# Performance work log

Hardware: AMD Instinct MI355X
Metric: run time of the kernel (lower is better)

## Reference

```python
import jax, jax.numpy as jnp
import numpy as np
import math

E = 1024
H = 16
D = E // H  # head_dim = 64
B, T = 2, 2048


def setup_inputs() -> dict:
    key = jax.random.key(0)
    ks = jax.random.split(key, 10)
    s_in = 1.0 / math.sqrt(E)
    s_hd = 1.0 / math.sqrt(D)
    return {
        "hidden_states": jax.random.normal(ks[0], (B, T, E), dtype=jnp.float32),
        # stacked per-head Linear weights (torch Linear: y = x @ W.T + b)
        "Wq": jax.random.uniform(ks[1], (H, E, D), jnp.float32, -s_in, s_in),
        "bq": jax.random.uniform(ks[2], (H, D), jnp.float32, -s_in, s_in),
        "Wk": jax.random.uniform(ks[3], (H, E, D), jnp.float32, -s_in, s_in),
        "bk": jax.random.uniform(ks[4], (H, D), jnp.float32, -s_in, s_in),
        "Wv": jax.random.uniform(ks[5], (H, E, D), jnp.float32, -s_in, s_in),
        "bv": jax.random.uniform(ks[6], (H, D), jnp.float32, -s_in, s_in),
        "Wo": jax.random.uniform(ks[7], (H, D, E), jnp.float32, -s_hd, s_hd),
        "bo": jax.random.uniform(ks[8], (H, E), jnp.float32, -s_hd, s_hd),
        "gate": jnp.ones((H,), dtype=jnp.float32),
    }


def reference(hidden_states, Wq, bq, Wk, bk, Wv, bv, Wo, bo, gate):
    # Batched per-head projections: [B,T,E] x [H,E,D] -> [B,H,T,D]
    Q = jnp.einsum("bte,hed->bhtd", hidden_states, Wq) + bq[None, :, None, :]
    K = jnp.einsum("bte,hed->bhtd", hidden_states, Wk) + bk[None, :, None, :]
    V = jnp.einsum("bte,hed->bhtd", hidden_states, Wv) + bv[None, :, None, :]
    scale = 1.0 / math.sqrt(D)
    scores = jnp.einsum("bhtd,bhsd->bhts", Q, K) * scale  # [B,H,T,T]
    weights = jax.nn.softmax(scores, axis=-1)
    attn = jnp.einsum("bhts,bhsd->bhtd", weights, V)  # [B,H,T,D]
    # Per-head output proj (bias included before gating), gated, summed over heads
    proj = jnp.einsum("bhtd,hde->bhte", attn, Wo) + bo[None, :, None, :]
    out = jnp.sum(proj * gate[None, :, None, None], axis=1)  # [B,T,E]
    return out
```

## Files before the change

### kernel.cpp

```cpp
#include <hip/hip_runtime.h>
#include <math.h>

#define E_DIM 1024
#define H_DIM 16
#define D_DIM 64
#define B_DIM 2
#define T_DIM 2048
#define M_TOT (B_DIM * T_DIM)

typedef __bf16 bf16_t;
typedef bf16_t bf16x4 __attribute__((ext_vector_type(4)));
typedef bf16_t bf16x8 __attribute__((ext_vector_type(8)));
typedef float f32x4 __attribute__((ext_vector_type(4)));

#define LOG2E_DIV8 0.18033688011112042f

__device__ __forceinline__ float fast_exp2(float x) {
#if __has_builtin(__builtin_amdgcn_exp2f)
    return __builtin_amdgcn_exp2f(x);
#else
    return __expf(x * 0.6931471805599453f);
#endif
}

__device__ __forceinline__ void load_lds16(const void* g, void* l) {
    __builtin_amdgcn_global_load_lds(
        (const __attribute__((address_space(1))) unsigned int*)g,
        (__attribute__((address_space(3))) unsigned int*)l, 16, 0, 0);
}

__global__ __launch_bounds__(256) void cast_x_kernel(const float* __restrict__ x,
                                                     bf16_t* __restrict__ xb) {
    size_t i = ((size_t)blockIdx.x * 256 + threadIdx.x) * 8;
    float4 a = *reinterpret_cast<const float4*>(x + i);
    float4 b = *reinterpret_cast<const float4*>(x + i + 4);
    bf16x8 o;
    o[0] = (bf16_t)a.x; o[1] = (bf16_t)a.y; o[2] = (bf16_t)a.z; o[3] = (bf16_t)a.w;
    o[4] = (bf16_t)b.x; o[5] = (bf16_t)b.y; o[6] = (bf16_t)b.z; o[7] = (bf16_t)b.w;
    *reinterpret_cast<bf16x8*>(xb + i) = o;
}

__global__ __launch_bounds__(256) void wqkv_t_kernel(
    const float* __restrict__ Wq, const float* __restrict__ Wk,
    const float* __restrict__ Wv, bf16_t* __restrict__ Wcat) {
    const int et = blockIdx.x, h = blockIdx.y, z = blockIdx.z;
    const float* W = z == 0 ? Wq : (z == 1 ? Wk : Wv);
    __shared__ float Tt[64][65];
    const int tid = threadIdx.x;
    const int r = tid >> 2, c4 = (tid & 3) * 16;
    const float* src = W + (size_t)h * 65536 + (size_t)(et * 64 + r) * 64 + c4;
    #pragma unroll
    for (int k = 0; k < 16; k += 4) {
        float4 v = *reinterpret_cast<const float4*>(src + k);
        Tt[r][c4 + k + 0] = v.x; Tt[r][c4 + k + 1] = v.y;
        Tt[r][c4 + k + 2] = v.z; Tt[r][c4 + k + 3] = v.w;
    }
    __syncthreads();
    bf16x8 o0, o1;
    #pragma unroll
    for (int k = 0; k < 8; ++k) o0[k] = (bf16_t)Tt[c4 + k][r];
    #pragma unroll
    for (int k = 0; k < 8; ++k) o1[k] = (bf16_t)Tt[c4 + 8 + k][r];
    bf16_t* dst = Wcat + ((size_t)(z * 16 + h) * 64 + r) * 1024 + et * 64 + c4;
    *reinterpret_cast<bf16x8*>(dst) = o0;
    *reinterpret_cast<bf16x8*>(dst + 8) = o1;
}

__global__ __launch_bounds__(256) void wo_t_kernel(const float* __restrict__ Wo,
                                                   const float* __restrict__ gate,
                                                   bf16_t* __restrict__ Wgt) {
    const int et = blockIdx.x, h = blockIdx.y;
    const float g = gate[h];
    __shared__ float Tt[64][65];
    const int tid = threadIdx.x;
    const int r = tid >> 2, c4 = (tid & 3) * 16;
    const float* src = Wo + (size_t)h * 65536 + (size_t)r * 1024 + et * 64 + c4;
    #pragma unroll
    for (int k = 0; k < 16; k += 4) {
        float4 v = *reinterpret_cast<const float4*>(src + k);
        Tt[r][c4 + k + 0] = v.x * g; Tt[r][c4 + k + 1] = v.y * g;
        Tt[r][c4 + k + 2] = v.z * g; Tt[r][c4 + k + 3] = v.w * g;
    }
    __syncthreads();
    bf16x8 o0, o1;
    #pragma unroll
    for (int k = 0; k < 8; ++k) o0[k] = (bf16_t)Tt[c4 + k][r];
    #pragma unroll
    for (int k = 0; k < 8; ++k) o1[k] = (bf16_t)Tt[c4 + 8 + k][r];
    bf16_t* dst = Wgt + (size_t)(et * 64 + r) * 1024 + h * 64 + c4;
    *reinterpret_cast<bf16x8*>(dst) = o0;
    *reinterpret_cast<bf16x8*>(dst + 8) = o1;
}

__global__ __launch_bounds__(256) void bias_sum_kernel(const float* __restrict__ bo,
                                                       const float* __restrict__ gate,
                                                       float* __restrict__ bsum) {
    int e = blockIdx.x * 256 + threadIdx.x;
    float s = 0.f;
    #pragma unroll
    for (int h = 0; h < H_DIM; ++h) s += gate[h] * bo[h * E_DIM + e];
    bsum[e] = s;
}

__global__ __launch_bounds__(256) void qk_gemm_kernel(
    const bf16_t* __restrict__ Xb, const bf16_t* __restrict__ Wcat,
    const float* __restrict__ bqp, const float* __restrict__ bkp,
    bf16_t* __restrict__ Qw, bf16_t* __restrict__ Kw) {
    const int p = blockIdx.x;
    const int l = (p & 7) * 64 + (p >> 3);
    const int mx = l & 31, ny = l >> 5;
    const int m0 = mx * 128, n0 = ny * 128;

    __shared__ bf16_t As[2][128][32];
    __shared__ bf16_t Bs[2][128][32];

    const int tid = threadIdx.x;
    const int lane = tid & 63, wid = tid >> 6;
    const int wr = wid >> 1, wc = wid & 1;
    const int lr = lane & 15, lg = lane >> 4;
    const int srow = lane >> 2, scol = (lane & 3) * 8;

    f32x4 acc[4][4] = {};

    #define STAGE_QK(buf, k0)                                                      \
        _Pragma("unroll")                                                          \
        for (int j = 0; j < 2; ++j) {                                              \
            load_lds16(Xb + (size_t)(m0 + wid * 32 + j * 16 + srow) * E_DIM + (k0) + scol, \
                       (char*)&As[buf][0][0] + wid * 2048 + j * 1024);             \
            load_lds16(Wcat + (size_t)(n0 + wid * 32 + j * 16 + srow) * E_DIM + (k0) + scol, \
                       (char*)&Bs[buf][0][0] + wid * 2048 + j * 1024);             \
        }

    STAGE_QK(0, 0);
    for (int t = 0; t < 32; ++t) {
        __syncthreads();
        if (t < 31) STAGE_QK((t + 1) & 1, (t + 1) * 32);
        const int b = t & 1;
        bf16x8 a[4], bb[4];
        #pragma unroll
        for (int i = 0; i < 4; ++i)
            a[i] = *reinterpret_cast<const bf16x8*>(&As[b][wr * 64 + i * 16 + lr][lg * 8]);
        #pragma unroll
        for (int j = 0; j < 4; ++j)
            bb[j] = *reinterpret_cast<const bf16x8*>(&Bs[b][wc * 64 + j * 16 + lr][lg * 8]);
        __builtin_amdgcn_s_setprio(1);
        #pragma unroll
        for (int j = 0; j < 4; ++j)
            #pragma unroll
            for (int i = 0; i < 4; ++i)
                acc[j][i] = __builtin_amdgcn_mfma_f32_16x16x32_bf16(bb[j], a[i], acc[j][i], 0, 0, 0);
        __builtin_amdgcn_s_setprio(0);
    }
    #undef STAGE_QK

    const int z = n0 >> 10;
    const float scale = (z == 0) ? LOG2E_DIV8 : 1.0f;
    const float* bias = (z == 0) ? bqp : bkp;
    bf16_t* Obase = (z == 0) ? Qw : Kw;
    const int b_idx = m0 >> 11;
    const int t00 = m0 & (T_DIM - 1);

    #pragma unroll
    for (int j = 0; j < 4; ++j) {
        const int n = n0 + wc * 64 + j * 16 + lg * 4;
        const int h = (n >> 6) & 15;
        const int dbase = (n & 63);
        const float4 bv4 = *reinterpret_cast<const float4*>(&bias[n & 1023]);
        bf16_t* O = Obase + (size_t)(b_idx * H_DIM + h) * T_DIM * 64;
        #pragma unroll
        for (int i = 0; i < 4; ++i) {
            const int t = t00 + wr * 64 + i * 16 + lr;
            bf16x4 t4;
            #pragma unroll
            for (int r = 0; r < 4; ++r)
                t4[r] = (bf16_t)((acc[j][i][r] + (&bv4.x)[r]) * scale);
            *reinterpret_cast<bf16x4*>(&O[(size_t)t * 64 + dbase]) = t4;
        }
    }
}

__global__ __launch_bounds__(256) void v_gemm_kernel(
    const bf16_t* __restrict__ Xb, const bf16_t* __restrict__ Wcat,
    const float* __restrict__ bvp, bf16_t* __restrict__ Vtw) {
    const int p = blockIdx.x;
    const int l = (p & 7) * 32 + (p >> 3);
    const int mx = l & 31, ny = l >> 5;
    const int m0 = mx * 128, n0 = ny * 128;
    const bf16_t* Wv = Wcat + (size_t)2048 * E_DIM;

    __shared__ bf16_t As[2][128][32];
    __shared__ bf16_t Bs[2][128][32];

    const int tid = threadIdx.x;
    const int lane = tid & 63, wid = tid >> 6;
    const int wr = wid >> 1, wc = wid & 1;
    const int lr = lane & 15, lg = lane >> 4;
    const int srow = lane >> 2, scol = (lane & 3) * 8;

    f32x4 acc[4][4] = {};

    #define STAGE_V(buf, k0)                                                       \
        _Pragma("unroll")                                                          \
        for (int j = 0; j < 2; ++j) {                                              \
            load_lds16(Xb + (size_t)(m0 + wid * 32 + j * 16 + srow) * E_DIM + (k0) + scol, \
                       (char*)&As[buf][0][0] + wid * 2048 + j * 1024);             \
            load_lds16(Wv + (size_t)(n0 + wid * 32 + j * 16 + srow) * E_DIM + (k0) + scol, \
                       (char*)&Bs[buf][0][0] + wid * 2048 + j * 1024);             \
        }

    STAGE_V(0, 0);
    for (int t = 0; t < 32; ++t) {
        __syncthreads();
        if (t < 31) STAGE_V((t + 1) & 1, (t + 1) * 32);
        const int b = t & 1;
        bf16x8 a[4], bb[4];
        #pragma unroll
        for (int i = 0; i < 4; ++i)
            a[i] = *reinterpret_cast<const bf16x8*>(&As[b][wr * 64 + i * 16 + lr][lg * 8]);
        #pragma unroll
        for (int j = 0; j < 4; ++j)
            bb[j] = *reinterpret_cast<const bf16x8*>(&Bs[b][wc * 64 + j * 16 + lr][lg * 8]);
        __builtin_amdgcn_s_setprio(1);
        #pragma unroll
        for (int i = 0; i < 4; ++i)
            #pragma unroll
            for (int j = 0; j < 4; ++j)
                acc[i][j] = __builtin_amdgcn_mfma_f32_16x16x32_bf16(a[i], bb[j], acc[i][j], 0, 0, 0);
        __builtin_amdgcn_s_setprio(0);
    }
    #undef STAGE_V

    const int b_idx = m0 >> 11;
    const int t00 = m0 & (T_DIM - 1);
    #pragma unroll
    for (int j = 0; j < 4; ++j) {
        const int n = n0 + wc * 64 + j * 16 + lr;
        const int h = (n >> 6) & 15;
        const int d = n & 63;
        const float bval = bvp[n];
        bf16_t* O = Vtw + (size_t)(b_idx * H_DIM + h) * 64 * T_DIM + (size_t)d * T_DIM;
        #pragma unroll
        for (int i = 0; i < 4; ++i) {
            const int t = t00 + wr * 64 + i * 16 + lg * 4;
            bf16x4 t4;
            #pragma unroll
            for (int r = 0; r < 4; ++r) t4[r] = (bf16_t)(acc[i][j][r] + bval);
            *reinterpret_cast<bf16x4*>(&O[t]) = t4;
        }
    }
}

__global__ __launch_bounds__(512, 4) void attn_mfma_kernel(
    const bf16_t* __restrict__ Q, const bf16_t* __restrict__ K,
    const bf16_t* __restrict__ Vt, bf16_t* __restrict__ Aw) {
    const int p = blockIdx.x;
    const int l = (p & 7) * 64 + (p >> 3);
    const int qx = l & 15, bh = l >> 4;
    const int b_idx = bh >> 4, h = bh & 15;
    const int q0 = qx * 128;
    const size_t base = (size_t)bh * T_DIM * 64;
    const int tstart = (qx & 1) << 3;

    __shared__ bf16_t Ks[128][72];
    __shared__ bf16_t Vs[64][136];
    __shared__ bf16_t Ps[8][16][136];

    const int tid = threadIdx.x;
    const int lane = tid & 63;
    const int wid = tid >> 6;
    const int lr = lane & 15, lg = lane >> 4;

    bf16x8 bq[2];
    #pragma unroll
    for (int kc = 0; kc < 2; ++kc)
        bq[kc] = *reinterpret_cast<const bf16x8*>(
            Q + base + (size_t)(q0 + wid * 16 + lr) * 64 + kc * 32 + lg * 8);

    const int kr = tid >> 2, kc0 = (tid & 3) * 16;
    const int vr = tid >> 3, vc0 = (tid & 7) * 16;

    bf16x8 kA, kB, vA, vB;
    {
        const bf16_t* ksrc = K + base + (size_t)(tstart * 128 + kr) * 64 + kc0;
        kA = *reinterpret_cast<const bf16x8*>(ksrc);
        kB = *reinterpret_cast<const bf16x8*>(ksrc + 8);
        const bf16_t* vsrc = Vt + base + (size_t)vr * T_DIM + tstart * 128 + vc0;
        vA = *reinterpret_cast<const bf16x8*>(vsrc);
        vB = *reinterpret_cast<const bf16x8*>(vsrc + 8);
        *reinterpret_cast<bf16x8*>(&Ks[kr][kc0])     = kA;
        *reinterpret_cast<bf16x8*>(&Ks[kr][kc0 + 8]) = kB;
        *reinterpret_cast<bf16x8*>(&Vs[vr][vc0])     = vA;
        *reinterpret_cast<bf16x8*>(&Vs[vr][vc0 + 8]) = vB;
    }
    __syncthreads();

    float mreg = -INFINITY, lrow = 0.f;
    f32x4 o[4] = {};

    for (int it = 0; it < 16; ++it) {
        const bool more = (it + 1) < 16;
        if (more) {
            const int nt = (tstart + it + 1) & 15;
            const bf16_t* ksrc = K + base + (size_t)(nt * 128 + kr) * 64 + kc0;
            kA = *reinterpret_cast<const bf16x8*>(ksrc);
            kB = *reinterpret_cast<const bf16x8*>(ksrc + 8);
            const bf16_t* vsrc = Vt + base + (size_t)vr * T_DIM + nt * 128 + vc0;
            vA = *reinterpret_cast<const bf16x8*>(vsrc);
            vB = *reinterpret_cast<const bf16x8*>(vsrc + 8);
        }

        f32x4 s[8] = {};
        __builtin_amdgcn_s_setprio(1);
        #pragma unroll
        for (int kb = 0; kb < 8; ++kb)
            #pragma unroll
            for (int kc = 0; kc < 2; ++kc) {
                bf16x8 ak = *reinterpret_cast<const bf16x8*>(&Ks[kb * 16 + lr][kc * 32 + lg * 8]);
                s[kb] = __builtin_amdgcn_mfma_f32_16x16x32_bf16(ak, bq[kc], s[kb], 0, 0, 0);
            }
        __builtin_amdgcn_s_setprio(0);

        float pmax = -INFINITY;
        #pragma unroll
        for (int kb = 0; kb < 8; ++kb)
            pmax = fmaxf(pmax,
                   fmaxf(fmaxf(s[kb][0], s[kb][1]), fmaxf(s[kb][2], s[kb][3])));
        pmax = fmaxf(pmax, __shfl_xor(pmax, 16));
        pmax = fmaxf(pmax, __shfl_xor(pmax, 32));

        if (__any(pmax > mreg + 11.5f)) {
            float newm = fmaxf(mreg, pmax);
            float alpha = fast_exp2(mreg - newm);
            mreg = newm;
            lrow *= alpha;
            #pragma unroll
            for (int db = 0; db < 4; ++db) o[db] *= alpha;
        }

        float rs = 0.f;
        #pragma unroll
        for (int kb = 0; kb < 8; ++kb) {
            bf16x4 t4;
            #pragma unroll
            for (int r = 0; r < 4; ++r) {
                float pv = fast_exp2(s[kb][r] - mreg);
                rs += pv;
                t4[r] = (bf16_t)pv;
            }
            *reinterpret_cast<bf16x4*>(&Ps[wid][lr][kb * 16 + lg * 4]) = t4;
        }
        rs += __shfl_xor(rs, 16);
        rs += __shfl_xor(rs, 32);
        lrow += rs;

        __builtin_amdgcn_s_setprio(1);
        #pragma unroll
        for (int sc = 0; sc < 4; ++sc) {
            bf16x8 bp = *reinterpret_cast<const bf16x8*>(&Ps[wid][lr][sc * 32 + lg * 8]);
            #pragma unroll
            for (int db = 0; db < 4; ++db) {
                bf16x8 av = *reinterpret_cast<const bf16x8*>(&Vs[db * 16 + lr][sc * 32 + lg * 8]);
                o[db] = __builtin_amdgcn_mfma_f32_16x16x32_bf16(av, bp, o[db], 0, 0, 0);
            }
        }
        __builtin_amdgcn_s_setprio(0);
        __syncthreads();

        if (more) {
            *reinterpret_cast<bf16x8*>(&Ks[kr][kc0])     = kA;
            *reinterpret_cast<bf16x8*>(&Ks[kr][kc0 + 8]) = kB;
            *reinterpret_cast<bf16x8*>(&Vs[vr][vc0])     = vA;
            *reinterpret_cast<bf16x8*>(&Vs[vr][vc0 + 8]) = vB;
        }
        __syncthreads();
    }

    const float linv = 1.f / lrow;
    const int t = q0 + wid * 16 + lr;
    const size_t rowbase = ((size_t)b_idx * T_DIM + t) * E_DIM + h * 64;
    #pragma unroll
    for (int db = 0; db < 4; ++db) {
        bf16x4 t4;
        #pragma unroll
        for (int r = 0; r < 4; ++r) t4[r] = (bf16_t)(o[db][r] * linv);
        *reinterpret_cast<bf16x4*>(&Aw[rowbase + db * 16 + lg * 4]) = t4;
    }
}

__global__ __launch_bounds__(256) void out_gemm_kernel(
    const bf16_t* __restrict__ Aw, const bf16_t* __restrict__ Wgt,
    const float* __restrict__ bsum, float* __restrict__ out) {
    const int p = blockIdx.x;
    const int l = (p & 7) * 32 + (p >> 3);
    const int mx = l & 31, ny = l >> 5;
    const int m0 = mx * 128, n0 = ny * 128;

    __shared__ bf16_t As[2][128][32];
    __shared__ bf16_t Bs[2][128][32];

    const int tid = threadIdx.x;
    const int lane = tid & 63, wid = tid >> 6;
    const int wr = wid >> 1, wc = wid & 1;
    const int lr = lane & 15, lg = lane >> 4;
    const int srow = lane >> 2, scol = (lane & 3) * 8;

    f32x4 acc[4][4] = {};

    #define STAGE_O(buf, k0)                                                       \
        _Pragma("unroll")                                                          \
        for (int j = 0; j < 2; ++j) {                                              \
            load_lds16(Aw + (size_t)(m0 + wid * 32 + j * 16 + srow) * E_DIM + (k0) + scol, \
                       (char*)&As[buf][0][0] + wid * 2048 + j * 1024);             \
            load_lds16(Wgt + (size_t)(n0 + wid * 32 + j * 16 + srow) * E_DIM + (k0) + scol, \
                       (char*)&Bs[buf][0][0] + wid * 2048 + j * 1024);             \
        }

    STAGE_O(0, 0);
    for (int t = 0; t < 32; ++t) {
        __syncthreads();
        if (t < 31) STAGE_O((t + 1) & 1, (t + 1) * 32);
        const int b = t & 1;
        bf16x8 a[4], bb[4];
        #pragma unroll
        for (int i = 0; i < 4; ++i)
            a[i] = *reinterpret_cast<const bf16x8*>(&As[b][wr * 64 + i * 16 + lr][lg * 8]);
        #pragma unroll
        for (int j = 0; j < 4; ++j)
            bb[j] = *reinterpret_cast<const bf16x8*>(&Bs[b][wc * 64 + j * 16 + lr][lg * 8]);
        __builtin_amdgcn_s_setprio(1);
        #pragma unroll
        for (int j = 0; j < 4; ++j)
            #pragma unroll
            for (int i = 0; i < 4; ++i)
                acc[j][i] = __builtin_amdgcn_mfma_f32_16x16x32_bf16(bb[j], a[i], acc[j][i], 0, 0, 0);
        __builtin_amdgcn_s_setprio(0);
    }
    #undef STAGE_O

    #pragma unroll
    for (int j = 0; j < 4; ++j) {
        const int e = n0 + wc * 64 + j * 16 + lg * 4;
        const float4 bs4 = *reinterpret_cast<const float4*>(&bsum[e]);
        #pragma unroll
        for (int i = 0; i < 4; ++i) {
            const int m = m0 + wr * 64 + i * 16 + lr;
            float4 o4;
            o4.x = acc[j][i][0] + bs4.x;
            o4.y = acc[j][i][1] + bs4.y;
            o4.z = acc[j][i][2] + bs4.z;
            o4.w = acc[j][i][3] + bs4.w;
            *reinterpret_cast<float4*>(&out[(size_t)m * E_DIM + e]) = o4;
        }
    }
}

extern "C" void kernel_launch(void* const* d_in, const int* in_sizes, int n_in,
                              void* d_out, int out_size, void* d_ws, size_t ws_size,
                              hipStream_t stream) {
    const float* hs   = (const float*)d_in[0];
    const float* Wq   = (const float*)d_in[1];
    const float* bq   = (const float*)d_in[2];
    const float* Wk   = (const float*)d_in[3];
    const float* bk   = (const float*)d_in[4];
    const float* Wv   = (const float*)d_in[5];
    const float* bv   = (const float*)d_in[6];
    const float* Wo   = (const float*)d_in[7];
    const float* bo   = (const float*)d_in[8];
    const float* gate = (const float*)d_in[9];
    float* out = (float*)d_out;

    const size_t NX = (size_t)M_TOT * E_DIM;
    const size_t NW = (size_t)H_DIM * D_DIM * E_DIM;
    bf16_t* p = (bf16_t*)d_ws;
    bf16_t* Xb   = p; p += NX;
    bf16_t* Wcat = p; p += 3 * NW;
    bf16_t* Wgt  = p; p += NW;
    bf16_t* Qw   = p; p += NX;
    bf16_t* Kw   = p; p += NX;
    bf16_t* Vtw  = p; p += NX;
    bf16_t* Aw   = p; p += NX;
    float*  bsum = (float*)p;

    cast_x_kernel<<<dim3(NX / 2048), 256, 0, stream>>>(hs, Xb);
    wqkv_t_kernel<<<dim3(16, 16, 3), 256, 0, stream>>>(Wq, Wk, Wv, Wcat);
    wo_t_kernel<<<dim3(16, 16), 256, 0, stream>>>(Wo, gate, Wgt);
    bias_sum_kernel<<<dim3(4), 256, 0, stream>>>(bo, gate, bsum);

    qk_gemm_kernel<<<dim3(512), 256, 0, stream>>>(Xb, Wcat, bq, bk, Qw, Kw);
    v_gemm_kernel<<<dim3(256), 256, 0, stream>>>(Xb, Wcat, bv, Vtw);

    attn_mfma_kernel<<<dim3(512), 512, 0, stream>>>(Qw, Kw, Vtw, Aw);

    out_gemm_kernel<<<dim3(256), 256, 0, stream>>>(Aw, Wgt, bsum, out);
}
```

Measured before the change: 245.8 us.

## Merge prep kernels, fuse QKV GEMMs, single-buffer LDS, halve out-GEMM tile

Folds the four preprocessing kernels into one launch that branches on block index, and merges the QK and V projection GEMMs into a single 768-block launch. It also drops the LDS double-buffering in the GEMMs in favour of single-buffered loads with two barriers per step. The attention kernel's register prefetch and staggered start tile are removed, and the output GEMM moves to 128x64 tiles so it launches 512 blocks. The goal is less launch overhead and better occupancy and SM fill, at the cost of no longer overlapping global loads with MFMA compute.

```diff
diff --git a/kernel.cpp b/kernel.cpp
--- a/kernel.cpp
+++ b/kernel.cpp
@@ -29,90 +29,91 @@
         (__attribute__((address_space(3))) unsigned int*)l, 16, 0, 0);
 }
 
-__global__ __launch_bounds__(256) void cast_x_kernel(const float* __restrict__ x,
-                                                     bf16_t* __restrict__ xb) {
-    size_t i = ((size_t)blockIdx.x * 256 + threadIdx.x) * 8;
-    float4 a = *reinterpret_cast<const float4*>(x + i);
-    float4 b = *reinterpret_cast<const float4*>(x + i + 4);
-    bf16x8 o;
-    o[0] = (bf16_t)a.x; o[1] = (bf16_t)a.y; o[2] = (bf16_t)a.z; o[3] = (bf16_t)a.w;
-    o[4] = (bf16_t)b.x; o[5] = (bf16_t)b.y; o[6] = (bf16_t)b.z; o[7] = (bf16_t)b.w;
-    *reinterpret_cast<bf16x8*>(xb + i) = o;
-}
-
-__global__ __launch_bounds__(256) void wqkv_t_kernel(
+__global__ __launch_bounds__(256) void prep_kernel(
+    const float* __restrict__ x,
     const float* __restrict__ Wq, const float* __restrict__ Wk,
-    const float* __restrict__ Wv, bf16_t* __restrict__ Wcat) {
-    const int et = blockIdx.x, h = blockIdx.y, z = blockIdx.z;
-    const float* W = z == 0 ? Wq : (z == 1 ? Wk : Wv);
+    const float* __restrict__ Wv, const float* __restrict__ Wo,
+    const float* __restrict__ bo, const float* __restrict__ gate,
+    bf16_t* __restrict__ Xb, bf16_t* __restrict__ Wcat,
+    bf16_t* __restrict__ Wgt, float* __restrict__ bsum) {
     __shared__ float Tt[64][65];
+    const int b = blockIdx.x;
     const int tid = threadIdx.x;
-    const int r = tid >> 2, c4 = (tid & 3) * 16;
-    const float* src = W + (size_t)h * 65536 + (size_t)(et * 64 + r) * 64 + c4;
-    #pragma unroll
-    for (int k = 0; k < 16; k += 4) {
-        float4 v = *reinterpret_cast<const float4*>(src + k);
-        Tt[r][c4 + k + 0] = v.x; Tt[r][c4 + k + 1] = v.y;
-        Tt[r][c4 + k + 2] = v.z; Tt[r][c4 + k + 3] = v.w;
-    }
-    __syncthreads();
-    bf16x8 o0, o1;
-    #pragma unroll
-    for (int k = 0; k < 8; ++k) o0[k] = (bf16_t)Tt[c4 + k][r];
-    #pragma unroll
-    for (int k = 0; k < 8; ++k) o1[k] = (bf16_t)Tt[c4 + 8 + k][r];
-    bf16_t* dst = Wcat + ((size_t)(z * 16 + h) * 64 + r) * 1024 + et * 64 + c4;
-    *reinterpret_cast<bf16x8*>(dst) = o0;
-    *reinterpret_cast<bf16x8*>(dst + 8) = o1;
-}
-
-__global__ __launch_bounds__(256) void wo_t_kernel(const float* __restrict__ Wo,
-                                                   const float* __restrict__ gate,
-                                                   bf16_t* __restrict__ Wgt) {
-    const int et = blockIdx.x, h = blockIdx.y;
-    const float g = gate[h];
-    __shared__ float Tt[64][65];
-    const int tid = threadIdx.x;
-    const int r = tid >> 2, c4 = (tid & 3) * 16;
-    const float* src = Wo + (size_t)h * 65536 + (size_t)r * 1024 + et * 64 + c4;
-    #pragma unroll
-    for (int k = 0; k < 16; k += 4) {
-        float4 v = *reinterpret_cast<const float4*>(src + k);
-        Tt[r][c4 + k + 0] = v.x * g; Tt[r][c4 + k + 1] = v.y * g;
-        Tt[r][c4 + k + 2] = v.z * g; Tt[r][c4 + k + 3] = v.w * g;
-    }
-    __syncthreads();
-    bf16x8 o0, o1;
-    #pragma unroll
-    for (int k = 0; k < 8; ++k) o0[k] = (bf16_t)Tt[c4 + k][r];
-    #pragma unroll
-    for (int k = 0; k < 8; ++k) o1[k] = (bf16_t)Tt[c4 + 8 + k][r];
-    bf16_t* dst = Wgt + (size_t)(et * 64 + r) * 1024 + h * 64 + c4;
-    *reinterpret_cast<bf16x8*>(dst) = o0;
-    *reinterpret_cast<bf16x8*>(dst + 8) = o1;
-}
-
-__global__ __launch_bounds__(256) void bias_sum_kernel(const float* __restrict__ bo,
-                                                       const float* __restrict__ gate,
-                                                       float* __restrict__ bsum) {
-    int e = blockIdx.x * 256 + threadIdx.x;
-    float s = 0.f;
-    #pragma unroll
-    for (int h = 0; h < H_DIM; ++h) s += gate[h] * bo[h * E_DIM + e];
-    bsum[e] = s;
-}
-
-__global__ __launch_bounds__(256) void qk_gemm_kernel(
+
+    if (b < 2048) {
+        size_t i = ((size_t)b * 256 + tid) * 8;
+        float4 a0 = *reinterpret_cast<const float4*>(x + i);
+        float4 a1 = *reinterpret_cast<const float4*>(x + i + 4);
+        bf16x8 o;
+        o[0] = (bf16_t)a0.x; o[1] = (bf16_t)a0.y; o[2] = (bf16_t)a0.z; o[3] = (bf16_t)a0.w;
+        o[4] = (bf16_t)a1.x; o[5] = (bf16_t)a1.y; o[6] = (bf16_t)a1.z; o[7] = (bf16_t)a1.w;
+        *reinterpret_cast<bf16x8*>(Xb + i) = o;
+    } else if (b < 2816) {
+        const int idx = b - 2048;
+        const int z = idx >> 8;
+        const int rem = idx & 255;
+        const int h = rem >> 4, et = rem & 15;
+        const float* W = z == 0 ? Wq : (z == 1 ? Wk : Wv);
+        const int r = tid >> 2, c4 = (tid & 3) * 16;
+        const float* src = W + (size_t)h * 65536 + (size_t)(et * 64 + r) * 64 + c4;
+        #pragma unroll
+        for (int k = 0; k < 16; k += 4) {
+            float4 v = *reinterpret_cast<const float4*>(src + k);
+            Tt[r][c4 + k + 0] = v.x; Tt[r][c4 + k + 1] = v.y;
+            Tt[r][c4 + k + 2] = v.z; Tt[r][c4 + k + 3] = v.w;
+        }
+        __syncthreads();
+        bf16x8 o0, o1;
+        #pragma unroll
+        for (int k = 0; k < 8; ++k) o0[k] = (bf16_t)Tt[c4 + k][r];
+        #pragma unroll
+        for (int k = 0; k < 8; ++k) o1[k] = (bf16_t)Tt[c4 + 8 + k][r];
+        bf16_t* dst = Wcat + ((size_t)(z * 16 + h) * 64 + r) * 1024 + et * 64 + c4;
+        *reinterpret_cast<bf16x8*>(dst) = o0;
+        *reinterpret_cast<bf16x8*>(dst + 8) = o1;
+    } else if (b < 3072) {
+        const int idx = b - 2816;
+        const int h = idx >> 4, et = idx & 15;
+        const float g = gate[h];
+        const int r = tid >> 2, c4 = (tid & 3) * 16;
+        const float* src = Wo + (size_t)h * 65536 + (size_t)r * 1024 + et * 64 + c4;
+        #pragma unroll
+        for (int k = 0; k < 16; k += 4) {
+            float4 v = *reinterpret_cast<const float4*>(src + k);
+            Tt[r][c4 + k + 0] = v.x * g; Tt[r][c4 + k + 1] = v.y * g;
+            Tt[r][c4 + k + 2] = v.z * g; Tt[r][c4 + k + 3] = v.w * g;
+        }
+        __syncthreads();
+        bf16x8 o0, o1;
+        #pragma unroll
+        for (int k = 0; k < 8; ++k) o0[k] = (bf16_t)Tt[c4 + k][r];
+        #pragma unroll
+        for (int k = 0; k < 8; ++k) o1[k] = (bf16_t)Tt[c4 + 8 + k][r];
+        bf16_t* dst = Wgt + (size_t)(et * 64 + r) * 1024 + h * 64 + c4;
+        *reinterpret_cast<bf16x8*>(dst) = o0;
+        *reinterpret_cast<bf16x8*>(dst + 8) = o1;
+    } else {
+        const int e = (b - 3072) * 256 + tid;
+        float s = 0.f;
+        #pragma unroll
+        for (int h = 0; h < H_DIM; ++h) s += gate[h] * bo[h * E_DIM + e];
+        bsum[e] = s;
+    }
+}
+
+__global__ __launch_bounds__(256) void qkv_gemm_kernel(
     const bf16_t* __restrict__ Xb, const bf16_t* __restrict__ Wcat,
     const float* __restrict__ bqp, const float* __restrict__ bkp,
-    bf16_t* __restrict__ Qw, bf16_t* __restrict__ Kw) {
+    const float* __restrict__ bvp,
+    bf16_t* __restrict__ Qw, bf16_t* __restrict__ Kw, bf16_t* __restrict__ Vtw) {
     const int p = blockIdx.x;
-    const int l = (p & 7) * 64 + (p >> 3);
+    const int l = (p & 7) * 96 + (p >> 3);
     const int mx = l & 31, ny = l >> 5;
     const int m0 = mx * 128, n0 = ny * 128;
-
-    __shared__ bf16_t As[2][128][32];
-    __shared__ bf16_t Bs[2][128][32];
+    const int z = n0 >> 10;
+
+    __shared__ bf16_t As[128][32];
+    __shared__ bf16_t Bs[128][32];
 
     const int tid = threadIdx.x;
     const int lane = tid & 63, wid = tid >> 6;
@@ -120,134 +121,95 @@
     const int lr = lane & 15, lg = lane >> 4;
     const int srow = lane >> 2, scol = (lane & 3) * 8;
 
-    f32x4 acc[4][4] = {};
-
-    #define STAGE_QK(buf, k0)                                                      \
+    const int b_idx = m0 >> 11;
+    const int t00 = m0 & (T_DIM - 1);
+
+    #define QKV_STAGE(k0)                                                          \
         _Pragma("unroll")                                                          \
         for (int j = 0; j < 2; ++j) {                                              \
             load_lds16(Xb + (size_t)(m0 + wid * 32 + j * 16 + srow) * E_DIM + (k0) + scol, \
-                       (char*)&As[buf][0][0] + wid * 2048 + j * 1024);             \
+                       (char*)&As[0][0] + wid * 2048 + j * 1024);                  \
             load_lds16(Wcat + (size_t)(n0 + wid * 32 + j * 16 + srow) * E_DIM + (k0) + scol, \
-                       (char*)&Bs[buf][0][0] + wid * 2048 + j * 1024);             \
-        }
-
-    STAGE_QK(0, 0);
-    for (int t = 0; t < 32; ++t) {
-        __syncthreads();
-        if (t < 31) STAGE_QK((t + 1) & 1, (t + 1) * 32);
-        const int b = t & 1;
-        bf16x8 a[4], bb[4];
-        #pragma unroll
-        for (int i = 0; i < 4; ++i)
-            a[i] = *reinterpret_cast<const bf16x8*>(&As[b][wr * 64 + i * 16 + lr][lg * 8]);
-        #pragma unroll
-        for (int j = 0; j < 4; ++j)
-            bb[j] = *reinterpret_cast<const bf16x8*>(&Bs[b][wc * 64 + j * 16 + lr][lg * 8]);
-        __builtin_amdgcn_s_setprio(1);
-        #pragma unroll
-        for (int j = 0; j < 4; ++j)
+                       (char*)&Bs[0][0] + wid * 2048 + j * 1024);                  \
+        }
+    #define QKV_FRAGS                                                              \
+        bf16x8 a[4], bb[4];                                                        \
+        _Pragma("unroll")                                                          \
+        for (int i = 0; i < 4; ++i)                                                \
+            a[i] = *reinterpret_cast<const bf16x8*>(&As[wr * 64 + i * 16 + lr][lg * 8]); \
+        _Pragma("unroll")                                                          \
+        for (int j = 0; j < 4; ++j)                                                \
+            bb[j] = *reinterpret_cast<const bf16x8*>(&Bs[wc * 64 + j * 16 + lr][lg * 8]);
+
+    if (z < 2) {
+        f32x4 acc[4][4] = {};
+        for (int k0 = 0; k0 < E_DIM; k0 += 32) {
+            QKV_STAGE(k0);
+            __syncthreads();
+            QKV_FRAGS;
+            __builtin_amdgcn_s_setprio(1);
+            #pragma unroll
+            for (int j = 0; j < 4; ++j)
+                #pragma unroll
+                for (int i = 0; i < 4; ++i)
+                    acc[j][i] = __builtin_amdgcn_mfma_f32_16x16x32_bf16(bb[j], a[i], acc[j][i], 0, 0, 0);
+            __builtin_amdgcn_s_setprio(0);
+            __syncthreads();
+        }
+        const float scale = (z == 0) ? LOG2E_DIV8 : 1.0f;
+        const float* bias = (z == 0) ? bqp : bkp;
+        bf16_t* Obase = (z == 0) ? Qw : Kw;
+        #pragma unroll
+        for (int j = 0; j < 4; ++j) {
+            const int n = n0 + wc * 64 + j * 16 + lg * 4;
+            const int h = (n >> 6) & 15;
+            const int dbase = n & 63;
+            const float4 bv4 = *reinterpret_cast<const float4*>(&bias[n & 1023]);
+            bf16_t* O = Obase + (size_t)(b_idx * H_DIM + h) * T_DIM * 64;
+            #pragma unroll
+            for (int i = 0; i < 4; ++i) {
+                const int t = t00 + wr * 64 + i * 16 + lr;
+                bf16x4 t4;
+                #pragma unroll
+                for (int r = 0; r < 4; ++r)
+                    t4[r] = (bf16_t)((acc[j][i][r] + (&bv4.x)[r]) * scale);
+                *reinterpret_cast<bf16x4*>(&O[(size_t)t * 64 + dbase]) = t4;
+            }
+        }
+    } else {
+        f32x4 acc[4][4] = {};
+        for (int k0 = 0; k0 < E_DIM; k0 += 32) {
+            QKV_STAGE(k0);
+            __syncthreads();
+            QKV_FRAGS;
+            __builtin_amdgcn_s_setprio(1);
             #pragma unroll
             for (int i = 0; i < 4; ++i)
-                acc[j][i] = __builtin_amdgcn_mfma_f32_16x16x32_bf16(bb[j], a[i], acc[j][i], 0, 0, 0);
-        __builtin_amdgcn_s_setprio(0);
-    }
-    #undef STAGE_QK
-
-    const int z = n0 >> 10;
-    const float scale = (z == 0) ? LOG2E_DIV8 : 1.0f;
-    const float* bias = (z == 0) ? bqp : bkp;
-    bf16_t* Obase = (z == 0) ? Qw : Kw;
-    const int b_idx = m0 >> 11;
-    const int t00 = m0 & (T_DIM - 1);
-
-    #pragma unroll
-    for (int j = 0; j < 4; ++j) {
-        const int n = n0 + wc * 64 + j * 16 + lg * 4;
-        const int h = (n >> 6) & 15;
-        const int dbase = (n & 63);
-        const float4 bv4 = *reinterpret_cast<const float4*>(&bias[n & 1023]);
-        bf16_t* O = Obase + (size_t)(b_idx * H_DIM + h) * T_DIM * 64;
-        #pragma unroll
-        for (int i = 0; i < 4; ++i) {
-            const int t = t00 + wr * 64 + i * 16 + lr;
-            bf16x4 t4;
-            #pragma unroll
-            for (int r = 0; r < 4; ++r)
-                t4[r] = (bf16_t)((acc[j][i][r] + (&bv4.x)[r]) * scale);
-            *reinterpret_cast<bf16x4*>(&O[(size_t)t * 64 + dbase]) = t4;
-        }
-    }
-}
-
-__global__ __launch_bounds__(256) void v_gemm_kernel(
-    const bf16_t* __restrict__ Xb, const bf16_t* __restrict__ Wcat,
-    const float* __restrict__ bvp, bf16_t* __restrict__ Vtw) {
-    const int p = blockIdx.x;
-    const int l = (p & 7) * 32 + (p >> 3);
-    const int mx = l & 31, ny = l >> 5;
-    const int m0 = mx * 128, n0 = ny * 128;
-    const bf16_t* Wv = Wcat + (size_t)2048 * E_DIM;
-
-    __shared__ bf16_t As[2][128][32];
-    __shared__ bf16_t Bs[2][128][32];
-
-    const int tid = threadIdx.x;
-    const int lane = tid & 63, wid = tid >> 6;
-    const int wr = wid >> 1, wc = wid & 1;
-    const int lr = lane & 15, lg = lane >> 4;
-    const int srow = lane >> 2, scol = (lane & 3) * 8;
-
-    f32x4 acc[4][4] = {};
-
-    #define STAGE_V(buf, k0)                                                       \
-        _Pragma("unroll")                                                          \
-        for (int j = 0; j < 2; ++j) {                                              \
-            load_lds16(Xb + (size_t)(m0 + wid * 32 + j * 16 + srow) * E_DIM + (k0) + scol, \
-                       (char*)&As[buf][0][0] + wid * 2048 + j * 1024);             \
-            load_lds16(Wv + (size_t)(n0 + wid * 32 + j * 16 + srow) * E_DIM + (k0) + scol, \
-                       (char*)&Bs[buf][0][0] + wid * 2048 + j * 1024);             \
-        }
-
-    STAGE_V(0, 0);
-    for (int t = 0; t < 32; ++t) {
-        __syncthreads();
-        if (t < 31) STAGE_V((t + 1) & 1, (t + 1) * 32);
-        const int b = t & 1;
-        bf16x8 a[4], bb[4];
-        #pragma unroll
-        for (int i = 0; i < 4; ++i)
-            a[i] = *reinterpret_cast<const bf16x8*>(&As[b][wr * 64 + i * 16 + lr][lg * 8]);
-        #pragma unroll
-        for (int j = 0; j < 4; ++j)
-            bb[j] = *reinterpret_cast<const bf16x8*>(&Bs[b][wc * 64 + j * 16 + lr][lg * 8]);
-        __builtin_amdgcn_s_setprio(1);
-        #pragma unroll
-        for (int i = 0; i < 4; ++i)
-            #pragma unroll
-            for (int j = 0; j < 4; ++j)
-                acc[i][j] = __builtin_amdgcn_mfma_f32_16x16x32_bf16(a[i], bb[j], acc[i][j], 0, 0, 0);
-        __builtin_amdgcn_s_setprio(0);
-    }
-    #undef STAGE_V
-
-    const int b_idx = m0 >> 11;
-    const int t00 = m0 & (T_DIM - 1);
-    #pragma unroll
-    for (int j = 0; j < 4; ++j) {
-        const int n = n0 + wc * 64 + j * 16 + lr;
-        const int h = (n >> 6) & 15;
-        const int d = n & 63;
-        const float bval = bvp[n];
-        bf16_t* O = Vtw + (size_t)(b_idx * H_DIM + h) * 64 * T_DIM + (size_t)d * T_DIM;
-        #pragma unroll
-        for (int i = 0; i < 4; ++i) {
-            const int t = t00 + wr * 64 + i * 16 + lg * 4;
-            bf16x4 t4;
-            #pragma unroll
-            for (int r = 0; r < 4; ++r) t4[r] = (bf16_t)(acc[i][j][r] + bval);
-            *reinterpret_cast<bf16x4*>(&O[t]) = t4;
-        }
-    }
+                #pragma unroll
+                for (int j = 0; j < 4; ++j)
+                    acc[i][j] = __builtin_amdgcn_mfma_f32_16x16x32_bf16(a[i], bb[j], acc[i][j], 0, 0, 0);
+            __builtin_amdgcn_s_setprio(0);
+            __syncthreads();
+        }
+        #pragma unroll
+        for (int j = 0; j < 4; ++j) {
+            const int n = n0 + wc * 64 + j * 16 + lr;
+            const int h = (n >> 6) & 15;
+            const int d = n & 63;
+            const float bval = bvp[n & 1023];
+            bf16_t* O = Vtw + (size_t)(b_idx * H_DIM + h) * 64 * T_DIM + (size_t)d * T_DIM;
+            #pragma unroll
+            for (int i = 0; i < 4; ++i) {
+                const int t = t00 + wr * 64 + i * 16 + lg * 4;
+                bf16x4 t4;
+                #pragma unroll
+                for (int r = 0; r < 4; ++r) t4[r] = (bf16_t)(acc[i][j][r] + bval);
+                *reinterpret_cast<bf16x4*>(&O[t]) = t4;
+            }
+        }
+    }
+    #undef QKV_STAGE
+    #undef QKV_FRAGS
 }
 
 __global__ __launch_bounds__(512, 4) void attn_mfma_kernel(
@@ -259,7 +221,6 @@
     const int b_idx = bh >> 4, h = bh & 15;
     const int q0 = qx * 128;
     const size_t base = (size_t)bh * T_DIM * 64;
-    const int tstart = (qx & 1) << 3;
 
     __shared__ bf16_t Ks[128][72];
     __shared__ bf16_t Vs[64][136];
@@ -279,35 +240,23 @@
     const int kr = tid >> 2, kc0 = (tid & 3) * 16;
     const int vr = tid >> 3, vc0 = (tid & 7) * 16;
 
-    bf16x8 kA, kB, vA, vB;
-    {
-        const bf16_t* ksrc = K + base + (size_t)(tstart * 128 + kr) * 64 + kc0;
-        kA = *reinterpret_cast<const bf16x8*>(ksrc);
-        kB = *reinterpret_cast<const bf16x8*>(ksrc + 8);
-        const bf16_t* vsrc = Vt + base + (size_t)vr * T_DIM + tstart * 128 + vc0;
-        vA = *reinterpret_cast<const bf16x8*>(vsrc);
-        vB = *reinterpret_cast<const bf16x8*>(vsrc + 8);
-        *reinterpret_cast<bf16x8*>(&Ks[kr][kc0])     = kA;
-        *reinterpret_cast<bf16x8*>(&Ks[kr][kc0 + 8]) = kB;
-        *reinterpret_cast<bf16x8*>(&Vs[vr][vc0])     = vA;
-        *reinterpret_cast<bf16x8*>(&Vs[vr][vc0 + 8]) = vB;
-    }
-    __syncthreads();
-
     float mreg = -INFINITY, lrow = 0.f;
     f32x4 o[4] = {};
 
-    for (int it = 0; it < 16; ++it) {
-        const bool more = (it + 1) < 16;
-        if (more) {
-            const int nt = (tstart + it + 1) & 15;
-            const bf16_t* ksrc = K + base + (size_t)(nt * 128 + kr) * 64 + kc0;
-            kA = *reinterpret_cast<const bf16x8*>(ksrc);
-            kB = *reinterpret_cast<const bf16x8*>(ksrc + 8);
-            const bf16_t* vsrc = Vt + base + (size_t)vr * T_DIM + nt * 128 + vc0;
-            vA = *reinterpret_cast<const bf16x8*>(vsrc);
-            vB = *reinterpret_cast<const bf16x8*>(vsrc + 8);
-        }
+    for (int s0 = 0; s0 < T_DIM; s0 += 128) {
+        {
+            const bf16_t* ksrc = K + base + (size_t)(s0 + kr) * 64 + kc0;
+            bf16x8 k0 = *reinterpret_cast<const bf16x8*>(ksrc);
+            bf16x8 k1 = *reinterpret_cast<const bf16x8*>(ksrc + 8);
+            const bf16_t* vsrc = Vt + base + (size_t)vr * T_DIM + s0 + vc0;
+            bf16x8 v0 = *reinterpret_cast<const bf16x8*>(vsrc);
+            bf16x8 v1 = *reinterpret_cast<const bf16x8*>(vsrc + 8);
+            *reinterpret_cast<bf16x8*>(&Ks[kr][kc0])     = k0;
+            *reinterpret_cast<bf16x8*>(&Ks[kr][kc0 + 8]) = k1;
+            *reinterpret_cast<bf16x8*>(&Vs[vr][vc0])     = v0;
+            *reinterpret_cast<bf16x8*>(&Vs[vr][vc0 + 8]) = v1;
+        }
+        __syncthreads();
 
         f32x4 s[8] = {};
         __builtin_amdgcn_s_setprio(1);
@@ -365,14 +314,6 @@
         }
         __builtin_amdgcn_s_setprio(0);
         __syncthreads();
-
-        if (more) {
-            *reinterpret_cast<bf16x8*>(&Ks[kr][kc0])     = kA;
-            *reinterpret_cast<bf16x8*>(&Ks[kr][kc0 + 8]) = kB;
-            *reinterpret_cast<bf16x8*>(&Vs[vr][vc0])     = vA;
-            *reinterpret_cast<bf16x8*>(&Vs[vr][vc0 + 8]) = vB;
-        }
-        __syncthreads();
     }
 
     const float linv = 1.f / lrow;
@@ -391,12 +332,12 @@
     const bf16_t* __restrict__ Aw, const bf16_t* __restrict__ Wgt,
     const float* __restrict__ bsum, float* __restrict__ out) {
     const int p = blockIdx.x;
-    const int l = (p & 7) * 32 + (p >> 3);
+    const int l = (p & 7) * 64 + (p >> 3);
     const int mx = l & 31, ny = l >> 5;
-    const int m0 = mx * 128, n0 = ny * 128;
-
-    __shared__ bf16_t As[2][128][32];
-    __shared__ bf16_t Bs[2][128][32];
+    const int m0 = mx * 128, n0 = ny * 64;
+
+    __shared__ bf16_t As[128][32];
+    __shared__ bf16_t Bs[64][32];
 
     const int tid = threadIdx.x;
     const int lane = tid & 63, wid = tid >> 6;
@@ -404,42 +345,36 @@
     const int lr = lane & 15, lg = lane >> 4;
     const int srow = lane >> 2, scol = (lane & 3) * 8;
 
-    f32x4 acc[4][4] = {};
-
-    #define STAGE_O(buf, k0)                                                       \
-        _Pragma("unroll")                                                          \
-        for (int j = 0; j < 2; ++j) {                                              \
-            load_lds16(Aw + (size_t)(m0 + wid * 32 + j * 16 + srow) * E_DIM + (k0) + scol, \
-                       (char*)&As[buf][0][0] + wid * 2048 + j * 1024);             \
-            load_lds16(Wgt + (size_t)(n0 + wid * 32 + j * 16 + srow) * E_DIM + (k0) + scol, \
-                       (char*)&Bs[buf][0][0] + wid * 2048 + j * 1024);             \
-        }
-
-    STAGE_O(0, 0);
-    for (int t = 0; t < 32; ++t) {
-        __syncthreads();
-        if (t < 31) STAGE_O((t + 1) & 1, (t + 1) * 32);
-        const int b = t & 1;
-        bf16x8 a[4], bb[4];
+    f32x4 acc[2][4] = {};
+
+    for (int k0 = 0; k0 < E_DIM; k0 += 32) {
+        #pragma unroll
+        for (int j = 0; j < 2; ++j)
+            load_lds16(Aw + (size_t)(m0 + wid * 32 + j * 16 + srow) * E_DIM + k0 + scol,
+                       (char*)&As[0][0] + wid * 2048 + j * 1024);
+        load_lds16(Wgt + (size_t)(n0 + wid * 16 + srow) * E_DIM + k0 + scol,
+                   (char*)&Bs[0][0] + wid * 1024);
+        __syncthreads();
+        bf16x8 a[4], bb[2];
         #pragma unroll
         for (int i = 0; i < 4; ++i)
-            a[i] = *reinterpret_cast<const bf16x8*>(&As[b][wr * 64 + i * 16 + lr][lg * 8]);
-        #pragma unroll
-        for (int j = 0; j < 4; ++j)
-            bb[j] = *reinterpret_cast<const bf16x8*>(&Bs[b][wc * 64 + j * 16 + lr][lg * 8]);
+            a[i] = *reinterpret_cast<const bf16x8*>(&As[wr * 64 + i * 16 + lr][lg * 8]);
+        #pragma unroll
+        for (int j = 0; j < 2; ++j)
+            bb[j] = *reinterpret_cast<const bf16x8*>(&Bs[wc * 32 + j * 16 + lr][lg * 8]);
         __builtin_amdgcn_s_setprio(1);
         #pragma unroll
-        for (int j = 0; j < 4; ++j)
+        for (int j = 0; j < 2; ++j)
             #pragma unroll
             for (int i = 0; i < 4; ++i)
                 acc[j][i] = __builtin_amdgcn_mfma_f32_16x16x32_bf16(bb[j], a[i], acc[j][i], 0, 0, 0);
         __builtin_amdgcn_s_setprio(0);
-    }
-    #undef STAGE_O
+        __syncthreads();
+    }
 
     #pragma unroll
-    for (int j = 0; j < 4; ++j) {
-        const int e = n0 + wc * 64 + j * 16 + lg * 4;
+    for (int j = 0; j < 2; ++j) {
+        const int e = n0 + wc * 32 + j * 16 + lg * 4;
         const float4 bs4 = *reinterpret_cast<const float4*>(&bsum[e]);
         #pragma unroll
         for (int i = 0; i < 4; ++i) {
@@ -481,15 +416,12 @@
     bf16_t* Aw   = p; p += NX;
     float*  bsum = (float*)p;
 
-    cast_x_kernel<<<dim3(NX / 2048), 256, 0, stream>>>(hs, Xb);
-    wqkv_t_kernel<<<dim3(16, 16, 3), 256, 0, stream>>>(Wq, Wk, Wv, Wcat);
-    wo_t_kernel<<<dim3(16, 16), 256, 0, stream>>>(Wo, gate, Wgt);
-    bias_sum_kernel<<<dim3(4), 256, 0, stream>>>(bo, gate, bsum);
-
-    qk_gemm_kernel<<<dim3(512), 256, 0, stream>>>(Xb, Wcat, bq, bk, Qw, Kw);
-    v_gemm_kernel<<<dim3(256), 256, 0, stream>>>(Xb, Wcat, bv, Vtw);
+    prep_kernel<<<dim3(3076), 256, 0, stream>>>(hs, Wq, Wk, Wv, Wo, bo, gate,
+                                                Xb, Wcat, Wgt, bsum);
+
+    qkv_gemm_kernel<<<dim3(768), 256, 0, stream>>>(Xb, Wcat, bq, bk, bv, Qw, Kw, Vtw);
 
     attn_mfma_kernel<<<dim3(512), 512, 0, stream>>>(Qw, Kw, Vtw, Aw);
 
-    out_gemm_kernel<<<dim3(256), 256, 0, stream>>>(Aw, Wgt, bsum, out);
-}
+    out_gemm_kernel<<<dim3(512), 256, 0, stream>>>(Aw, Wgt, bsum, out);
+}
```

After: 205.5 us. -16.4%, faster.
